# Performance work log

Measured on AMD Instinct MI355X. Metric: run time of the kernel, lower is better.

Reference implementation:

```python
import jax, jax.numpy as jnp
import numpy as np

IN_CH = 64
OUT_CH = 32
SCALE = 2
BLOCK = SCALE ** 3  # 8
N = 400000   # input sparse voxels (lines in pair_fwd)
M = 200000   # output sparse voxels


def setup_inputs() -> dict:
    key = jax.random.key(0)
    k1, k2, k3 = jax.random.split(key, 3)
    x_features = jax.random.normal(k1, (N, IN_CH), dtype=jnp.float32)
    # flat ParameterList: weights[i*BLOCK + j] is the (in_channels,) weight for
    # output channel i, kernel position j
    weights = jax.random.normal(k2, (BLOCK * OUT_CH, IN_CH), dtype=jnp.float32)
    # spconv pair_fwd: [kernel_volume, num_lines], -1 marks invalid mapping
    pair_fwd = jax.random.randint(k3, (BLOCK, N), -1, M)
    return {"x_features": x_features, "weights": weights,
            "pair_fwd": pair_fwd, "num_out": M}


def reference(x_features, weights, pair_fwd, num_out):
    block, n = pair_fwd.shape
    out_ch = weights.shape[0] // block
    # W[o, j, c] == weights_list[o*block + j]
    W = weights.reshape(out_ch, block, -1)
    # sequential VoxelShuffle then .view(-1) per block is identity on each
    # voxel's in_channels feature vector, so:
    # vals[j, n, o] = dot(W[o, j, :], x_features[n, :])
    vals = jnp.einsum('nc,ojc->jno', x_features, W)  # [block, N, out_ch]
    idx = pair_fwd.reshape(-1)                       # [block*N]
    # route invalid (-1) entries to a dummy trailing row
    safe = jnp.where(idx >= 0, idx, num_out)
    buf = jnp.zeros((num_out + 1, out_ch), dtype=vals.dtype)
    # original uses assignment (set) semantics into out_features
    buf = buf.at[safe].set(vals.reshape(block * n, out_ch))
    return buf[:num_out]
```

## Files before the change

### kernel.cpp

```cpp
#include <hip/hip_runtime.h>

#define IN_CH  64
#define OUT_CH 32
#define BLOCK  8

using short8 = __attribute__((ext_vector_type(8))) short;
using f32x4v = __attribute__((ext_vector_type(4))) float;


__global__ void k_prep(int4* __restrict__ argmax4, int n4, int4* __restrict__ claimed4, int nc4) {
    int i = blockIdx.x * 256 + threadIdx.x;
    if (i < n4) argmax4[i] = make_int4(-1, -1, -1, -1);
    if (i < nc4) claimed4[i] = make_int4(0, 0, 0, 0);
}

__global__ void k_scatter7(const int* __restrict__ pair, int* __restrict__ argmax,
                           unsigned char* __restrict__ claimed, int N) {
    int i = blockIdx.x * 256 + threadIdx.x;
    if (i >= N) return;
    int n = N - 1 - i;
    int t = 7 * N + n;
    int m = pair[t];
    if (m >= 0) {
        claimed[m] = 1;
        atomicMax(&argmax[m], t);
    }
}

__global__ void k_scatter_rest(const int* __restrict__ pair, int* __restrict__ argmax,
                               const unsigned char* __restrict__ claimed, int N) {
    int n = blockIdx.x * 256 + threadIdx.x;
    if (n >= N) return;
    for (int j = 6; j >= 0; --j) {
        int t = j * N + n;
        int m = pair[t];
        if (m >= 0 && !claimed[m] && argmax[m] < t)
            atomicMax(&argmax[m], t);
    }
}

__device__ __forceinline__ unsigned cvt_pk_bf16(float lo, float hi) {
    unsigned r;
    asm("v_cvt_pk_bf16_f32 %0, %1, %2" : "=v"(r) : "v"(lo), "v"(hi));
    return r;
}

__device__ __forceinline__ short8 pack8(float4 a, float4 b) {
    union { unsigned u[4]; short8 s; } p;
    p.u[0] = cvt_pk_bf16(a.x, a.y);
    p.u[1] = cvt_pk_bf16(a.z, a.w);
    p.u[2] = cvt_pk_bf16(b.x, b.y);
    p.u[3] = cvt_pk_bf16(b.z, b.w);
    return p.s;
}

__global__ __launch_bounds__(256, 4) void k_compute(
        const float* __restrict__ x, const float* __restrict__ w,
        const int* __restrict__ argmax, float* __restrict__ out,
        int M, int N) {
    const int lane = threadIdx.x & 63;
    const int r16  = lane & 15;
    const int kc   = lane >> 4;
    const int wv   = threadIdx.x >> 6;

    int base = (blockIdx.x * 4 + wv) * 64;
    if (base >= M) return;

    int t_[4];
#pragma unroll
    for (int st = 0; st < 4; ++st)
        t_[st] = argmax[base + st * 16 + r16];
    const int N1 = N, N2 = 2 * N, N4 = 4 * N;
    int j_[4], n_[4];
#pragma unroll
    for (int st = 0; st < 4; ++st) {
        int v = t_[st], j = 0;
        if (v >= N4) { j = 4;  v -= N4; }
        if (v >= N2) { j += 2; v -= N2; }
        if (v >= N1) { j += 1; v -= N1; }
        bool ok = t_[st] >= 0;
        j_[st] = ok ? j : 8;
        n_[st] = ok ? v : 0;
    }

    float4 xs[2][4];
    {
        const float* xp = x + (size_t)n_[0] * IN_CH + kc * 8;
        xs[0][0] = *(const float4*)xp;        xs[0][1] = *(const float4*)(xp + 4);
        xs[0][2] = *(const float4*)(xp + 32); xs[0][3] = *(const float4*)(xp + 36);
    }

#pragma unroll
    for (int st = 0; st < 4; ++st) {
        const int cur = st & 1;
        if (st < 3) {
            const float* xp = x + (size_t)n_[st + 1] * IN_CH + kc * 8;
            xs[cur ^ 1][0] = *(const float4*)xp;        xs[cur ^ 1][1] = *(const float4*)(xp + 4);
            xs[cur ^ 1][2] = *(const float4*)(xp + 32); xs[cur ^ 1][3] = *(const float4*)(xp + 36);
        }

        short8 a0 = pack8(xs[cur][0], xs[cur][1]);
        short8 a1 = pack8(xs[cur][2], xs[cur][3]);
        const int jr = j_[st];
        const short8 zz = (short8)0;

        f32x4v acc0 = {0.f, 0.f, 0.f, 0.f};
        f32x4v acc1 = {0.f, 0.f, 0.f, 0.f};
#pragma unroll
        for (int j = 0; j < 8; ++j) {
            bool pj = (jr == j);
            if (__ballot(pj) == 0ull) continue;
            short8 m0 = pj ? a0 : zz;
            short8 m1 = pj ? a1 : zz;
            const float* wp0 = w + ((r16)      * BLOCK + j) * IN_CH + kc * 8;
            const float* wp1 = w + ((16 + r16) * BLOCK + j) * IN_CH + kc * 8;
            short8 b00 = pack8(*(const float4*)wp0,        *(const float4*)(wp0 + 4));
            short8 b01 = pack8(*(const float4*)(wp0 + 32), *(const float4*)(wp0 + 36));
            short8 b10 = pack8(*(const float4*)wp1,        *(const float4*)(wp1 + 4));
            short8 b11 = pack8(*(const float4*)(wp1 + 32), *(const float4*)(wp1 + 36));
            acc0 = __builtin_amdgcn_mfma_f32_16x16x32_bf16(m0, b00, acc0, 0, 0, 0);
            acc0 = __builtin_amdgcn_mfma_f32_16x16x32_bf16(m1, b01, acc0, 0, 0, 0);
            acc1 = __builtin_amdgcn_mfma_f32_16x16x32_bf16(m0, b10, acc1, 0, 0, 0);
            acc1 = __builtin_amdgcn_mfma_f32_16x16x32_bf16(m1, b11, acc1, 0, 0, 0);
        }

#pragma unroll
        for (int q = 0; q < 4; ++q) {
            size_t ro = (size_t)(base + st * 16 + kc * 4 + q) * OUT_CH;
            out[ro + r16]      = acc0[q];
            out[ro + 16 + r16] = acc1[q];
        }
    }
}

extern "C" void kernel_launch(void* const* d_in, const int* in_sizes, int n_in,
                              void* d_out, int out_size, void* d_ws, size_t ws_size,
                              hipStream_t stream) {
    const float* x    = (const float*)d_in[0];
    const float* w    = (const float*)d_in[1];
    const int*   pair = (const int*)d_in[2];
    int N = in_sizes[0] / IN_CH;
    int M = out_size / OUT_CH;

    int*           argmax  = (int*)d_ws;
    unsigned char* claimed = (unsigned char*)d_ws + (size_t)M * 4;

    int n4  = M / 4;
    int nc4 = M / 16;
    k_prep<<<(n4 + 255) / 256, 256, 0, stream>>>((int4*)argmax, n4, (int4*)claimed, nc4);

    int gN = (N + 255) / 256;
    k_scatter7    <<<gN, 256, 0, stream>>>(pair, argmax, claimed, N);
    k_scatter_rest<<<gN, 256, 0, stream>>>(pair, argmax, claimed, N);

    int tiles  = M / 64;
    int blocks = (tiles + 3) / 4;
    k_compute<<<blocks, 256, 0, stream>>>(x, w, argmax, (float*)d_out, M, N);
}
```

Baseline: 91.30 us.

## Overlap scatter-rest with compute for kernel-7-claimed rows, defer rest to list

```diff
diff --git a/kernel.cpp b/kernel.cpp
--- a/kernel.cpp
+++ b/kernel.cpp
@@ -8,8 +8,10 @@
 using f32x4v = __attribute__((ext_vector_type(4))) float;
 
 
-__global__ void k_prep(int4* __restrict__ argmax4, int n4, int4* __restrict__ claimed4, int nc4) {
+__global__ void k_prep(int4* __restrict__ argmax4, int n4,
+                       int4* __restrict__ claimed4, int nc4, int* __restrict__ count) {
     int i = blockIdx.x * 256 + threadIdx.x;
+    if (i == 0) *count = 0;
     if (i < n4) argmax4[i] = make_int4(-1, -1, -1, -1);
     if (i < nc4) claimed4[i] = make_int4(0, 0, 0, 0);
 }
@@ -23,19 +25,7 @@
     int m = pair[t];
     if (m >= 0) {
         claimed[m] = 1;
-        atomicMax(&argmax[m], t);
-    }
-}
-
-__global__ void k_scatter_rest(const int* __restrict__ pair, int* __restrict__ argmax,
-                               const unsigned char* __restrict__ claimed, int N) {
-    int n = blockIdx.x * 256 + threadIdx.x;
-    if (n >= N) return;
-    for (int j = 6; j >= 0; --j) {
-        int t = j * N + n;
-        int m = pair[t];
-        if (m >= 0 && !claimed[m] && argmax[m] < t)
-            atomicMax(&argmax[m], t);
+        if (argmax[m] < t) atomicMax(&argmax[m], t);
     }
 }
 
@@ -54,10 +44,23 @@
     return p.s;
 }
 
-__global__ __launch_bounds__(256, 4) void k_compute(
+__global__ __launch_bounds__(256, 3) void k_mix(
         const float* __restrict__ x, const float* __restrict__ w,
-        const int* __restrict__ argmax, float* __restrict__ out,
-        int M, int N) {
+        const int* __restrict__ pair, int* __restrict__ argmax,
+        const unsigned char* __restrict__ claimed, float* __restrict__ out,
+        int* __restrict__ list, int* __restrict__ count,
+        int M, int N, int nA) {
+    if ((int)blockIdx.x >= nA) {
+        int n = (blockIdx.x - nA) * 256 + threadIdx.x;
+        if (n >= N) return;
+        for (int j = 6; j >= 0; --j) {
+            int t = j * N + n;
+            int m = pair[t];
+            if (m >= 0 && !claimed[m] && argmax[m] < t)
+                atomicMax(&argmax[m], t);
+        }
+        return;
+    }
     const int lane = threadIdx.x & 63;
     const int r16  = lane & 15;
     const int kc   = lane >> 4;
@@ -66,22 +69,41 @@
     int base = (blockIdx.x * 4 + wv) * 64;
     if (base >= M) return;
 
-    int t_[4];
+    const int TH = 7 * N;
+    int t_[4], n_[4];
+    bool cl[4];
 #pragma unroll
     for (int st = 0; st < 4; ++st)
         t_[st] = argmax[base + st * 16 + r16];
-    const int N1 = N, N2 = 2 * N, N4 = 4 * N;
-    int j_[4], n_[4];
 #pragma unroll
     for (int st = 0; st < 4; ++st) {
-        int v = t_[st], j = 0;
-        if (v >= N4) { j = 4;  v -= N4; }
-        if (v >= N2) { j += 2; v -= N2; }
-        if (v >= N1) { j += 1; v -= N1; }
-        bool ok = t_[st] >= 0;
-        j_[st] = ok ? j : 8;
-        n_[st] = ok ? v : 0;
-    }
+        cl[st] = (t_[st] >= TH);
+        n_[st] = cl[st] ? t_[st] - TH : 0;
+    }
+
+#pragma unroll
+    for (int st = 0; st < 4; ++st) {
+        unsigned long long ub = __ballot(!cl[st] && kc == 0);
+        if (ub) {
+            int leader = (int)__ffsll(ub) - 1;
+            int bp = 0;
+            if (lane == leader) bp = atomicAdd(count, __popcll(ub));
+            bp = __shfl(bp, leader);
+            if (!cl[st] && kc == 0) {
+                int pre = (int)__popcll(ub & ((1ull << lane) - 1ull));
+                list[bp + pre] = base + st * 16 + r16;
+            }
+        }
+    }
+
+    short8 bf7[2][2];
+#pragma unroll
+    for (int ot = 0; ot < 2; ++ot)
+#pragma unroll
+        for (int kk = 0; kk < 2; ++kk) {
+            const float* wp = w + ((ot * 16 + r16) * BLOCK + 7) * IN_CH + kk * 32 + kc * 8;
+            bf7[ot][kk] = pack8(*(const float4*)wp, *(const float4*)(wp + 4));
+        }
 
     float4 xs[2][4];
     {
@@ -98,22 +120,75 @@
             xs[cur ^ 1][0] = *(const float4*)xp;        xs[cur ^ 1][1] = *(const float4*)(xp + 4);
             xs[cur ^ 1][2] = *(const float4*)(xp + 32); xs[cur ^ 1][3] = *(const float4*)(xp + 36);
         }
-
         short8 a0 = pack8(xs[cur][0], xs[cur][1]);
         short8 a1 = pack8(xs[cur][2], xs[cur][3]);
-        const int jr = j_[st];
-        const short8 zz = (short8)0;
 
         f32x4v acc0 = {0.f, 0.f, 0.f, 0.f};
         f32x4v acc1 = {0.f, 0.f, 0.f, 0.f};
-#pragma unroll
-        for (int j = 0; j < 8; ++j) {
-            bool pj = (jr == j);
+        acc0 = __builtin_amdgcn_mfma_f32_16x16x32_bf16(a0, bf7[0][0], acc0, 0, 0, 0);
+        acc0 = __builtin_amdgcn_mfma_f32_16x16x32_bf16(a1, bf7[0][1], acc0, 0, 0, 0);
+        acc1 = __builtin_amdgcn_mfma_f32_16x16x32_bf16(a0, bf7[1][0], acc1, 0, 0, 0);
+        acc1 = __builtin_amdgcn_mfma_f32_16x16x32_bf16(a1, bf7[1][1], acc1, 0, 0, 0);
+
+        unsigned long long cb = __ballot(cl[st]);
+#pragma unroll
+        for (int q = 0; q < 4; ++q) {
+            int r = kc * 4 + q;
+            if ((cb >> r) & 1ull) {
+                size_t ro = (size_t)(base + st * 16 + r) * OUT_CH;
+                out[ro + r16]      = acc0[q];
+                out[ro + 16 + r16] = acc1[q];
+            }
+        }
+    }
+}
+
+__global__ __launch_bounds__(256, 4) void k_computeB(
+        const float* __restrict__ x, const float* __restrict__ w,
+        const int* __restrict__ argmax, const int* __restrict__ list,
+        const int* __restrict__ count, float* __restrict__ out, int M, int N) {
+    const int lane = threadIdx.x & 63;
+    const int r16  = lane & 15;
+    const int kc   = lane >> 4;
+    const int wv   = threadIdx.x >> 6;
+
+    int cnt  = *count;
+    int nsub = (cnt + 15) >> 4;
+    int gw   = blockIdx.x * 4 + wv;
+    int nw   = gridDim.x * 4;
+    const int N1 = N, N2 = 2 * N, N4 = 4 * N;
+
+    for (int s = gw; s < nsub; s += nw) {
+        int  li  = s * 16 + r16;
+        bool ok  = li < cnt;
+        int  idx = ok ? list[li] : 0;
+        int  t   = ok ? argmax[idx] : -1;
+        int v = t, j = 0;
+        if (v >= N4) { j = 4;  v -= N4; }
+        if (v >= N2) { j += 2; v -= N2; }
+        if (v >= N1) { j += 1; v -= N1; }
+        int jr = (t >= 0) ? j : 8;
+        int n  = (t >= 0) ? v : 0;
+
+        const float* xp = x + (size_t)n * IN_CH + kc * 8;
+        float4 x0 = *(const float4*)xp;
+        float4 x1 = *(const float4*)(xp + 4);
+        float4 x2 = *(const float4*)(xp + 32);
+        float4 x3 = *(const float4*)(xp + 36);
+        short8 a0 = pack8(x0, x1);
+        short8 a1 = pack8(x2, x3);
+        const short8 zz = (short8)0;
+
+        f32x4v acc0 = {0.f, 0.f, 0.f, 0.f};
+        f32x4v acc1 = {0.f, 0.f, 0.f, 0.f};
+#pragma unroll
+        for (int j2 = 0; j2 < 7; ++j2) {
+            bool pj = (jr == j2);
             if (__ballot(pj) == 0ull) continue;
             short8 m0 = pj ? a0 : zz;
             short8 m1 = pj ? a1 : zz;
-            const float* wp0 = w + ((r16)      * BLOCK + j) * IN_CH + kc * 8;
-            const float* wp1 = w + ((16 + r16) * BLOCK + j) * IN_CH + kc * 8;
+            const float* wp0 = w + ((r16)      * BLOCK + j2) * IN_CH + kc * 8;
+            const float* wp1 = w + ((16 + r16) * BLOCK + j2) * IN_CH + kc * 8;
             short8 b00 = pack8(*(const float4*)wp0,        *(const float4*)(wp0 + 4));
             short8 b01 = pack8(*(const float4*)(wp0 + 32), *(const float4*)(wp0 + 36));
             short8 b10 = pack8(*(const float4*)wp1,        *(const float4*)(wp1 + 4));
@@ -124,11 +199,16 @@
             acc1 = __builtin_amdgcn_mfma_f32_16x16x32_bf16(m1, b11, acc1, 0, 0, 0);
         }
 
+        unsigned long long okb = __ballot(ok);
 #pragma unroll
         for (int q = 0; q < 4; ++q) {
-            size_t ro = (size_t)(base + st * 16 + kc * 4 + q) * OUT_CH;
-            out[ro + r16]      = acc0[q];
-            out[ro + 16 + r16] = acc1[q];
+            int r = kc * 4 + q;
+            if ((okb >> r) & 1ull) {
+                int idxr = __shfl(idx, r);
+                size_t ro = (size_t)idxr * OUT_CH;
+                out[ro + r16]      = acc0[q];
+                out[ro + 16 + r16] = acc1[q];
+            }
         }
     }
 }
@@ -142,18 +222,23 @@
     int N = in_sizes[0] / IN_CH;
     int M = out_size / OUT_CH;
 
-    int*           argmax  = (int*)d_ws;
-    unsigned char* claimed = (unsigned char*)d_ws + (size_t)M * 4;
+    char*          ws      = (char*)d_ws;
+    int*           argmax  = (int*)ws;
+    unsigned char* claimed = (unsigned char*)(ws + (size_t)M * 4);
+    int*           count   = (int*)(ws + (size_t)M * 5);
+    int*           list    = (int*)(ws + (size_t)M * 5 + 256);
 
     int n4  = M / 4;
     int nc4 = M / 16;
-    k_prep<<<(n4 + 255) / 256, 256, 0, stream>>>((int4*)argmax, n4, (int4*)claimed, nc4);
+    k_prep<<<(n4 + 255) / 256, 256, 0, stream>>>((int4*)argmax, n4, (int4*)claimed, nc4, count);
 
     int gN = (N + 255) / 256;
-    k_scatter7    <<<gN, 256, 0, stream>>>(pair, argmax, claimed, N);
-    k_scatter_rest<<<gN, 256, 0, stream>>>(pair, argmax, claimed, N);
-
-    int tiles  = M / 64;
-    int blocks = (tiles + 3) / 4;
-    k_compute<<<blocks, 256, 0, stream>>>(x, w, argmax, (float*)d_out, M, N);
-}
+    k_scatter7<<<gN, 256, 0, stream>>>(pair, argmax, claimed, N);
+
+    int nA = (M / 64 + 3) / 4;
+    k_mix<<<nA + gN, 256, 0, stream>>>(x, w, pair, argmax, claimed,
+                                       (float*)d_out, list, count, M, N, nA);
+
+    k_computeB<<<512, 256, 0, stream>>>(x, w, argmax, list, count,
+                                        (float*)d_out, M, N);
+}
```

After: 214.2 us. +134.6%, slower.
